# Optimization experiments

Hardware: AMD Instinct MI355X
Metric: run time of the kernel (lower is better)

## Reference

```python
import jax, jax.numpy as jnp
import numpy as np

jax.config.update("jax_enable_x64", True)

P = 2038074743          # prime used by the ROBE-Z hash
BLOCK_K = 32            # tile sizes of the hashed reconstruction (kernel tile)
BLOCK_N = 32
INPUT_DIM = 8192
OUTPUT_DIM = 8192
HASH_SIZE = 1 << 22     # compressed parameter count
TOKENS = 512


def setup_inputs() -> dict:
    key = jax.random.key(0)
    k1, k2 = jax.random.split(key, 2)
    x = jax.random.normal(k1, (TOKENS, INPUT_DIM), dtype=jnp.float32)
    hashed_weight = jax.random.normal(k2, (HASH_SIZE,), dtype=jnp.float32) * 0.02
    bias = jnp.zeros((OUTPUT_DIM,), dtype=jnp.float32)
    # mirrors RzLinear._generate_random_numbers(seed): 4 random ints made even, prepended with P
    rng = np.random.RandomState(1024)
    r = rng.randint(0, P, size=(4,)).astype(np.int64)
    r = r + (r % 2)
    random_numbers = jnp.asarray(np.concatenate([np.array([P], dtype=np.int64), r]), dtype=jnp.int64)
    return {"x": x, "hashed_weight": hashed_weight, "bias": bias, "random_numbers": random_numbers}


def _weight_indices(random_numbers):
    """Hashed flat indices into hashed_weight for the dense [K, N] weight."""
    K, N = INPUT_DIM, OUTPUT_DIM
    kt, nt = K // BLOCK_K, N // BLOCK_N
    R1, R2, R3 = random_numbers[1], random_numbers[2], random_numbers[3]
    k_ids = jnp.arange(kt, dtype=jnp.int64)
    n_ids = jnp.arange(nt, dtype=jnp.int64)
    # per-tile start offset into the compressed array
    start = ((k_ids[:, None] * R3 + n_ids[None, :] * R2 + R1) % P) % (HASH_SIZE - BLOCK_K * BLOCK_N + 1)
    start = start.astype(jnp.int32)  # [kt, nt]
    off = (jnp.arange(BLOCK_K, dtype=jnp.int32)[:, None] * BLOCK_N
           + jnp.arange(BLOCK_N, dtype=jnp.int32)[None, :])  # [BK, BN], row-major within tile
    idx = start[:, None, :, None] + off[None, :, None, :]    # [kt, BK, nt, BN]
    return idx.reshape(K, N)


def reference(x, hashed_weight, bias, random_numbers):
    idx = _weight_indices(random_numbers)          # [K, N] int32
    W = hashed_weight[idx]                          # hashed-gather reconstruction, [K, N]
    out = jnp.matmul(x, W) + bias[None, :]          # [tokens, N]
    return out
```

## Files before the change

### kernel.cpp

```cpp
#include <hip/hip_runtime.h>
#include <hip/hip_fp16.h>

#define NDIM 8192
#define KDIM 8192
#define NT 256
#define MOD2 4193281
#define PRIME 2038074743LL

#define BM 256
#define BN 128
#define BK 32
#define KITER 64
#define ASTRIDE 40
#define BSLAB 1032

typedef _Float16 half8 __attribute__((ext_vector_type(8)));
typedef float floatx4 __attribute__((ext_vector_type(4)));

__global__ __launch_bounds__(256) void prep_kernel(const float* __restrict__ x,
                                                   const float* __restrict__ hw,
                                                   const float* __restrict__ bias,
                                                   const int* __restrict__ rn,
                                                   __half* __restrict__ xh,
                                                   __half* __restrict__ hh,
                                                   int* __restrict__ starts,
                                                   float* __restrict__ out) {
    int b = blockIdx.x;
    int tid = threadIdx.x;
    if (b < 8192) {
        int i = b * 256 + tid;
        const float4* s; __half2* d; int j;
        if (i < (1 << 20)) { s = (const float4*)x;  d = (__half2*)xh; j = i; }
        else               { s = (const float4*)hw; d = (__half2*)hh; j = i - (1 << 20); }
        float4 v = s[j];
        d[j * 2]     = __floats2half2_rn(v.x, v.y);
        d[j * 2 + 1] = __floats2half2_rn(v.z, v.w);
    } else if (b < 8192 + 4096) {
        int i = (b - 8192) * 256 + tid;
        float4 bv = *(const float4*)(bias + ((i & 2047) << 2));
        ((float4*)out)[i] = bv;
    } else {
        int t = (b - 12288) * 256 + tid;
        bool is64 = (rn[1] == 0 && rn[3] == 0);
        long long R1 = is64 ? rn[2] : rn[1];
        long long R2 = is64 ? rn[4] : rn[2];
        long long R3 = is64 ? rn[6] : rn[3];
        long long k_id = t >> 8, n_id = t & 255;
        long long v = (k_id * R3 + n_id * R2 + R1) % PRIME;
        starts[t] = (int)(v % MOD2);
    }
}

__global__ __launch_bounds__(512, 4) void gemm_kernel(
    const __half* __restrict__ xh, const __half* __restrict__ hh,
    const int* __restrict__ starts, float* __restrict__ out) {
    __shared__ __align__(16) __half As[2][BM * ASTRIDE];
    __shared__ __align__(16) __half Bs[2][4 * BSLAB];
    __shared__ int Ss[KITER * 4];

    const int tid = threadIdx.x;
    const int lane = tid & 63;
    const int wave = tid >> 6;
    const int wm = wave >> 1;
    const int wn = wave & 1;
    const int quad = lane >> 4;
    const int l16 = lane & 15;

    const int i = blockIdx.x;
    const int ks = i & 3;
    const int m_blk = (i >> 2) & 1;
    const int n_blk = i >> 3;
    const int gm0 = m_blk * BM;
    const int gn0 = n_blk * BN;
    const int kt0 = ks * KITER;
    const int n_id0 = n_blk * 4;

    if (tid < KITER * 4) {
        int kp = tid >> 2, tile = tid & 3;
        Ss[tid] = starts[(kt0 + kp) * NT + n_id0 + tile];
    }

    const int a_row = tid >> 2;
    const int a_ch = tid & 3;
    const __half* aptr = xh + (size_t)(gm0 + a_row) * KDIM + kt0 * 32 + a_ch * 8;
    const unsigned a_woff = a_row * ASTRIDE + a_ch * 8;

    const int b_tile = tid >> 7;
    const int t7 = tid & 127;
    const int b_np = t7 & 15;
    const int b_kg = t7 >> 4;
    const int b_oct = b_kg >> 1;
    const unsigned b_woff = b_oct * BSLAB + (b_tile * 32 + 2 * b_np) * 8 + (b_kg & 1) * 4;

    uint4 paA0, paA1, paB0, paB1;
    unsigned pbA0, pbA1, pbA2, pbA3, pbB0, pbB1, pbB2, pbB3;

#define LOADT(P0, P1, Q0, Q1, Q2, Q3, kp_) do {                                \
        P0 = *(const uint4*)(aptr + (kp_) * 32);                               \
        P1 = *(const uint4*)(aptr + (size_t)128 * KDIM + (kp_) * 32);          \
        int st = Ss[(kp_) * 4 + b_tile];                                       \
        const __half* src = hh + st + b_kg * 128 + b_np * 2;                   \
        Q0 = *(const unsigned*)(src);                                          \
        Q1 = *(const unsigned*)(src + 32);                                     \
        Q2 = *(const unsigned*)(src + 64);                                     \
        Q3 = *(const unsigned*)(src + 96);                                     \
    } while (0)

#define STORET(P0, P1, Q0, Q1, Q2, Q3, buf_) do {                              \
        *(uint4*)&As[buf_][a_woff] = P0;                                       \
        *(uint4*)&As[buf_][(a_woff) + 128 * ASTRIDE] = P1;                     \
        unsigned lo0 = (Q0 & 0xffffu) | (Q1 << 16);                            \
        unsigned lo1 = (Q2 & 0xffffu) | (Q3 << 16);                            \
        unsigned hi0 = (Q0 >> 16) | (Q1 & 0xffff0000u);                        \
        unsigned hi1 = (Q2 >> 16) | (Q3 & 0xffff0000u);                        \
        uint2 e = {lo0, lo1}, o = {hi0, hi1};                                  \
        *(uint2*)&Bs[buf_][b_woff] = e;                                        \
        *(uint2*)&Bs[buf_][b_woff + 8] = o;                                    \
    } while (0)

    floatx4 acc[4][4];
#pragma unroll
    for (int r = 0; r < 4; r++)
#pragma unroll
        for (int c = 0; c < 4; c++)
            acc[r][c] = (floatx4){0.f, 0.f, 0.f, 0.f};

#define FRAGS_MFMA(buf_) do {                                                  \
        half8 af[4], bf[4];                                                    \
        _Pragma("unroll")                                                      \
        for (int r = 0; r < 4; r++)                                            \
            af[r] = *(const half8*)&As[buf_][(wm * 64 + r * 16 + l16) * ASTRIDE + quad * 8]; \
        _Pragma("unroll")                                                      \
        for (int c = 0; c < 4; c++)                                            \
            bf[c] = *(const half8*)&Bs[buf_][quad * BSLAB + (wn * 64 + c * 16 + l16) * 8];   \
        _Pragma("unroll")                                                      \
        for (int r = 0; r < 4; r++)                                            \
            _Pragma("unroll")                                                  \
            for (int c = 0; c < 4; c++)                                        \
                acc[r][c] = __builtin_amdgcn_mfma_f32_16x16x32_f16(af[r], bf[c], acc[r][c], 0, 0, 0); \
    } while (0)

    __syncthreads();
    LOADT(paA0, paA1, pbA0, pbA1, pbA2, pbA3, 0);
    LOADT(paB0, paB1, pbB0, pbB1, pbB2, pbB3, 1);
    STORET(paA0, paA1, pbA0, pbA1, pbA2, pbA3, 0);
    __syncthreads();

    for (int kp = 0; kp < KITER; kp += 2) {
        if (kp + 2 < KITER) LOADT(paA0, paA1, pbA0, pbA1, pbA2, pbA3, kp + 2);
        FRAGS_MFMA(0);
        STORET(paB0, paB1, pbB0, pbB1, pbB2, pbB3, 1);
        __syncthreads();

        if (kp + 3 < KITER) LOADT(paB0, paB1, pbB0, pbB1, pbB2, pbB3, kp + 3);
        FRAGS_MFMA(1);
        if (kp + 2 < KITER)
            STORET(paA0, paA1, pbA0, pbA1, pbA2, pbA3, 0);
        __syncthreads();
    }

#pragma unroll
    for (int c = 0; c < 4; c++) {
        int col = gn0 + wn * 64 + c * 16 + l16;
#pragma unroll
        for (int r = 0; r < 4; r++) {
            int row0 = gm0 + wm * 64 + r * 16 + quad * 4;
#pragma unroll
            for (int e = 0; e < 4; e++)
                atomicAdd(&out[(size_t)(row0 + e) * NDIM + col], acc[r][c][e]);
        }
    }
#undef LOADT
#undef STORET
#undef FRAGS_MFMA
}

extern "C" void kernel_launch(void* const* d_in, const int* in_sizes, int n_in,
                              void* d_out, int out_size, void* d_ws, size_t ws_size,
                              hipStream_t stream) {
    const float* x = (const float*)d_in[0];
    const float* hw = (const float*)d_in[1];
    const float* bias = (const float*)d_in[2];
    const int* rn = (const int*)d_in[3];
    float* out = (float*)d_out;

    char* ws = (char*)d_ws;
    __half* xh = (__half*)ws;
    __half* hh = (__half*)(ws + (8u << 20));
    int* starts = (int*)(ws + (16u << 20));

    hipLaunchKernelGGL(prep_kernel, dim3(12544), dim3(256), 0, stream,
                       x, hw, bias, rn, xh, hh, starts, out);
    hipLaunchKernelGGL(gemm_kernel, dim3(512), dim3(512), 0, stream, xh, hh, starts, out);
}
```

Measured before the change: 202.4 us.

## Fuse fp32-to-fp16 conversion and hash start computation into GEMM loads

Removes the separate pass that converts x and the hashed weight to fp16 and precomputes tile start offsets. The GEMM now loads fp32 directly, packs to half when storing to shared memory, and computes each block's hash starts inline. This drops a full read and write of about 24 MB of converted data, but doubles global load bytes in the GEMM main loop and raises register pressure for the prefetch buffers.

```diff
diff --git a/kernel.cpp b/kernel.cpp
--- a/kernel.cpp
+++ b/kernel.cpp
@@ -17,43 +17,26 @@
 typedef _Float16 half8 __attribute__((ext_vector_type(8)));
 typedef float floatx4 __attribute__((ext_vector_type(4)));
 
-__global__ __launch_bounds__(256) void prep_kernel(const float* __restrict__ x,
-                                                   const float* __restrict__ hw,
-                                                   const float* __restrict__ bias,
-                                                   const int* __restrict__ rn,
-                                                   __half* __restrict__ xh,
-                                                   __half* __restrict__ hh,
-                                                   int* __restrict__ starts,
+__global__ __launch_bounds__(256) void prep_kernel(const float* __restrict__ bias,
                                                    float* __restrict__ out) {
-    int b = blockIdx.x;
-    int tid = threadIdx.x;
-    if (b < 8192) {
-        int i = b * 256 + tid;
-        const float4* s; __half2* d; int j;
-        if (i < (1 << 20)) { s = (const float4*)x;  d = (__half2*)xh; j = i; }
-        else               { s = (const float4*)hw; d = (__half2*)hh; j = i - (1 << 20); }
-        float4 v = s[j];
-        d[j * 2]     = __floats2half2_rn(v.x, v.y);
-        d[j * 2 + 1] = __floats2half2_rn(v.z, v.w);
-    } else if (b < 8192 + 4096) {
-        int i = (b - 8192) * 256 + tid;
-        float4 bv = *(const float4*)(bias + ((i & 2047) << 2));
-        ((float4*)out)[i] = bv;
-    } else {
-        int t = (b - 12288) * 256 + tid;
-        bool is64 = (rn[1] == 0 && rn[3] == 0);
-        long long R1 = is64 ? rn[2] : rn[1];
-        long long R2 = is64 ? rn[4] : rn[2];
-        long long R3 = is64 ? rn[6] : rn[3];
-        long long k_id = t >> 8, n_id = t & 255;
-        long long v = (k_id * R3 + n_id * R2 + R1) % PRIME;
-        starts[t] = (int)(v % MOD2);
-    }
+    int i = blockIdx.x * 256 + threadIdx.x;
+    float4 bv = *(const float4*)(bias + ((i & 2047) << 2));
+    ((float4*)out)[i] = bv;
 }
 
+__device__ inline unsigned pkh(float a, float b) {
+    __half2 h = __floats2half2_rn(a, b);
+    return *reinterpret_cast<unsigned*>(&h);
+}
+
+struct PF {
+    float4 a0, a1, a2, a3;
+    float2 b0, b1, b2, b3;
+};
+
 __global__ __launch_bounds__(512, 4) void gemm_kernel(
-    const __half* __restrict__ xh, const __half* __restrict__ hh,
-    const int* __restrict__ starts, float* __restrict__ out) {
+    const float* __restrict__ x, const float* __restrict__ hw,
+    const int* __restrict__ rn, float* __restrict__ out) {
     __shared__ __align__(16) __half As[2][BM * ASTRIDE];
     __shared__ __align__(16) __half Bs[2][4 * BSLAB];
     __shared__ int Ss[KITER * 4];
@@ -77,12 +60,18 @@
 
     if (tid < KITER * 4) {
         int kp = tid >> 2, tile = tid & 3;
-        Ss[tid] = starts[(kt0 + kp) * NT + n_id0 + tile];
+        bool is64 = (rn[1] == 0 && rn[3] == 0);
+        long long R1 = is64 ? rn[2] : rn[1];
+        long long R2 = is64 ? rn[4] : rn[2];
+        long long R3 = is64 ? rn[6] : rn[3];
+        long long k_id = kt0 + kp, n_id = n_id0 + tile;
+        long long v = (k_id * R3 + n_id * R2 + R1) % PRIME;
+        Ss[tid] = (int)(v % MOD2);
     }
 
     const int a_row = tid >> 2;
     const int a_ch = tid & 3;
-    const __half* aptr = xh + (size_t)(gm0 + a_row) * KDIM + kt0 * 32 + a_ch * 8;
+    const float* aptr = x + (size_t)(gm0 + a_row) * KDIM + kt0 * 32 + a_ch * 8;
     const unsigned a_woff = a_row * ASTRIDE + a_ch * 8;
 
     const int b_tile = tid >> 7;
@@ -92,28 +81,30 @@
     const int b_oct = b_kg >> 1;
     const unsigned b_woff = b_oct * BSLAB + (b_tile * 32 + 2 * b_np) * 8 + (b_kg & 1) * 4;
 
-    uint4 paA0, paA1, paB0, paB1;
-    unsigned pbA0, pbA1, pbA2, pbA3, pbB0, pbB1, pbB2, pbB3;
+    PF pfA, pfB;
 
-#define LOADT(P0, P1, Q0, Q1, Q2, Q3, kp_) do {                                \
-        P0 = *(const uint4*)(aptr + (kp_) * 32);                               \
-        P1 = *(const uint4*)(aptr + (size_t)128 * KDIM + (kp_) * 32);          \
+#define LOADT(P, kp_) do {                                                     \
+        P.a0 = *(const float4*)(aptr + (kp_) * 32);                            \
+        P.a1 = *(const float4*)(aptr + (kp_) * 32 + 4);                        \
+        P.a2 = *(const float4*)(aptr + (size_t)128 * KDIM + (kp_) * 32);       \
+        P.a3 = *(const float4*)(aptr + (size_t)128 * KDIM + (kp_) * 32 + 4);   \
         int st = Ss[(kp_) * 4 + b_tile];                                       \
-        const __half* src = hh + st + b_kg * 128 + b_np * 2;                   \
-        Q0 = *(const unsigned*)(src);                                          \
-        Q1 = *(const unsigned*)(src + 32);                                     \
-        Q2 = *(const unsigned*)(src + 64);                                     \
-        Q3 = *(const unsigned*)(src + 96);                                     \
+        const float* src = hw + st + b_kg * 128 + b_np * 2;                    \
+        P.b0 = *(const float2*)(src);                                          \
+        P.b1 = *(const float2*)(src + 32);                                     \
+        P.b2 = *(const float2*)(src + 64);                                     \
+        P.b3 = *(const float2*)(src + 96);                                     \
     } while (0)
 
-#define STORET(P0, P1, Q0, Q1, Q2, Q3, buf_) do {                              \
-        *(uint4*)&As[buf_][a_woff] = P0;                                       \
-        *(uint4*)&As[buf_][(a_woff) + 128 * ASTRIDE] = P1;                     \
-        unsigned lo0 = (Q0 & 0xffffu) | (Q1 << 16);                            \
-        unsigned lo1 = (Q2 & 0xffffu) | (Q3 << 16);                            \
-        unsigned hi0 = (Q0 >> 16) | (Q1 & 0xffff0000u);                        \
-        unsigned hi1 = (Q2 >> 16) | (Q3 & 0xffff0000u);                        \
-        uint2 e = {lo0, lo1}, o = {hi0, hi1};                                  \
+#define STORET(P, buf_) do {                                                   \
+        uint4 av0 = { pkh(P.a0.x, P.a0.y), pkh(P.a0.z, P.a0.w),                \
+                      pkh(P.a1.x, P.a1.y), pkh(P.a1.z, P.a1.w) };              \
+        uint4 av1 = { pkh(P.a2.x, P.a2.y), pkh(P.a2.z, P.a2.w),                \
+                      pkh(P.a3.x, P.a3.y), pkh(P.a3.z, P.a3.w) };              \
+        *(uint4*)&As[buf_][a_woff] = av0;                                      \
+        *(uint4*)&As[buf_][a_woff + 128 * ASTRIDE] = av1;                      \
+        uint2 e = { pkh(P.b0.x, P.b1.x), pkh(P.b2.x, P.b3.x) };                \
+        uint2 o = { pkh(P.b0.y, P.b1.y), pkh(P.b2.y, P.b3.y) };                \
         *(uint2*)&Bs[buf_][b_woff] = e;                                        \
         *(uint2*)&Bs[buf_][b_woff + 8] = o;                                    \
     } while (0)
@@ -141,21 +132,21 @@
     } while (0)
 
     __syncthreads();
-    LOADT(paA0, paA1, pbA0, pbA1, pbA2, pbA3, 0);
-    LOADT(paB0, paB1, pbB0, pbB1, pbB2, pbB3, 1);
-    STORET(paA0, paA1, pbA0, pbA1, pbA2, pbA3, 0);
+    LOADT(pfA, 0);
+    LOADT(pfB, 1);
+    STORET(pfA, 0);
     __syncthreads();
 
     for (int kp = 0; kp < KITER; kp += 2) {
-        if (kp + 2 < KITER) LOADT(paA0, paA1, pbA0, pbA1, pbA2, pbA3, kp + 2);
+        if (kp + 2 < KITER) LOADT(pfA, kp + 2);
         FRAGS_MFMA(0);
-        STORET(paB0, paB1, pbB0, pbB1, pbB2, pbB3, 1);
+        STORET(pfB, 1);
         __syncthreads();
 
-        if (kp + 3 < KITER) LOADT(paB0, paB1, pbB0, pbB1, pbB2, pbB3, kp + 3);
+        if (kp + 3 < KITER) LOADT(pfB, kp + 3);
         FRAGS_MFMA(1);
         if (kp + 2 < KITER)
-            STORET(paA0, paA1, pbA0, pbA1, pbA2, pbA3, 0);
+            STORET(pfA, 0);
         __syncthreads();
     }
 
@@ -183,13 +174,8 @@
     const float* bias = (const float*)d_in[2];
     const int* rn = (const int*)d_in[3];
     float* out = (float*)d_out;
+    (void)d_ws; (void)ws_size;
 
-    char* ws = (char*)d_ws;
-    __half* xh = (__half*)ws;
-    __half* hh = (__half*)(ws + (8u << 20));
-    int* starts = (int*)(ws + (16u << 20));
-
-    hipLaunchKernelGGL(prep_kernel, dim3(12544), dim3(256), 0, stream,
-                       x, hw, bias, rn, xh, hh, starts, out);
-    hipLaunchKernelGGL(gemm_kernel, dim3(512), dim3(512), 0, stream, xh, hh, starts, out);
+    hipLaunchKernelGGL(prep_kernel, dim3(4096), dim3(256), 0, stream, bias, out);
+    hipLaunchKernelGGL(gemm_kernel, dim3(512), dim3(512), 0, stream, x, hw, rn, out);
 }
```

Result: slower. 410.6 us (+102.9%).

## Shrink GEMM block to 128x128 tile with 4 waves and 2-way split-K

Applied to the files above, without the earlier changes.

Reshapes the GEMM decomposition from 256x128 tiles with 8 waves and 4-way split-K to 128x128 tiles with 4 waves and 2-way split-K over 128 k-tiles each. Each thread now loads twice as many B elements per stage and the start-table prefetch loops over threads. The aim is to halve the atomicAdd traffic on the output and allow more resident blocks per CU. In exchange, each B tile is fetched by four M-blocks instead of two, and each block runs a longer serial K loop.

```diff
diff --git a/kernel.cpp b/kernel.cpp
--- a/kernel.cpp
+++ b/kernel.cpp
@@ -7,10 +7,10 @@
 #define MOD2 4193281
 #define PRIME 2038074743LL
 
-#define BM 256
+#define BM 128
 #define BN 128
 #define BK 32
-#define KITER 64
+#define KITER 128
 #define ASTRIDE 40
 #define BSLAB 1032
 
@@ -51,7 +51,7 @@
     }
 }
 
-__global__ __launch_bounds__(512, 4) void gemm_kernel(
+__global__ __launch_bounds__(256, 4) void gemm_kernel(
     const __half* __restrict__ xh, const __half* __restrict__ hh,
     const int* __restrict__ starts, float* __restrict__ out) {
     __shared__ __align__(16) __half As[2][BM * ASTRIDE];
@@ -67,17 +67,17 @@
     const int l16 = lane & 15;
 
     const int i = blockIdx.x;
-    const int ks = i & 3;
-    const int m_blk = (i >> 2) & 1;
+    const int ks = i & 1;
+    const int m_blk = (i >> 1) & 3;
     const int n_blk = i >> 3;
     const int gm0 = m_blk * BM;
     const int gn0 = n_blk * BN;
     const int kt0 = ks * KITER;
     const int n_id0 = n_blk * 4;
 
-    if (tid < KITER * 4) {
-        int kp = tid >> 2, tile = tid & 3;
-        Ss[tid] = starts[(kt0 + kp) * NT + n_id0 + tile];
+    for (int s = tid; s < KITER * 4; s += 256) {
+        int kp = s >> 2, tile = s & 3;
+        Ss[s] = starts[(kt0 + kp) * NT + n_id0 + tile];
     }
 
     const int a_row = tid >> 2;
@@ -85,37 +85,49 @@
     const __half* aptr = xh + (size_t)(gm0 + a_row) * KDIM + kt0 * 32 + a_ch * 8;
     const unsigned a_woff = a_row * ASTRIDE + a_ch * 8;
 
-    const int b_tile = tid >> 7;
-    const int t7 = tid & 127;
-    const int b_np = t7 & 15;
-    const int b_kg = t7 >> 4;
+    const int b_tile = tid >> 6;
+    const int t6 = tid & 63;
+    const int b_np = t6 & 15;
+    const int b_kg = t6 >> 4;
     const int b_oct = b_kg >> 1;
     const unsigned b_woff = b_oct * BSLAB + (b_tile * 32 + 2 * b_np) * 8 + (b_kg & 1) * 4;
 
     uint4 paA0, paA1, paB0, paB1;
-    unsigned pbA0, pbA1, pbA2, pbA3, pbB0, pbB1, pbB2, pbB3;
-
-#define LOADT(P0, P1, Q0, Q1, Q2, Q3, kp_) do {                                \
+    unsigned pbA0, pbA1, pbA2, pbA3, pbA4, pbA5, pbA6, pbA7;
+    unsigned pbB0, pbB1, pbB2, pbB3, pbB4, pbB5, pbB6, pbB7;
+
+#define LOADT(P0, P1, Q0, Q1, Q2, Q3, Q4, Q5, Q6, Q7, kp_) do {                \
         P0 = *(const uint4*)(aptr + (kp_) * 32);                               \
-        P1 = *(const uint4*)(aptr + (size_t)128 * KDIM + (kp_) * 32);          \
+        P1 = *(const uint4*)(aptr + (size_t)64 * KDIM + (kp_) * 32);           \
         int st = Ss[(kp_) * 4 + b_tile];                                       \
         const __half* src = hh + st + b_kg * 128 + b_np * 2;                   \
         Q0 = *(const unsigned*)(src);                                          \
         Q1 = *(const unsigned*)(src + 32);                                     \
         Q2 = *(const unsigned*)(src + 64);                                     \
         Q3 = *(const unsigned*)(src + 96);                                     \
+        Q4 = *(const unsigned*)(src + 512);                                    \
+        Q5 = *(const unsigned*)(src + 544);                                    \
+        Q6 = *(const unsigned*)(src + 576);                                    \
+        Q7 = *(const unsigned*)(src + 608);                                    \
     } while (0)
 
-#define STORET(P0, P1, Q0, Q1, Q2, Q3, buf_) do {                              \
+#define STORET(P0, P1, Q0, Q1, Q2, Q3, Q4, Q5, Q6, Q7, buf_) do {              \
         *(uint4*)&As[buf_][a_woff] = P0;                                       \
-        *(uint4*)&As[buf_][(a_woff) + 128 * ASTRIDE] = P1;                     \
+        *(uint4*)&As[buf_][(a_woff) + 64 * ASTRIDE] = P1;                      \
         unsigned lo0 = (Q0 & 0xffffu) | (Q1 << 16);                            \
         unsigned lo1 = (Q2 & 0xffffu) | (Q3 << 16);                            \
         unsigned hi0 = (Q0 >> 16) | (Q1 & 0xffff0000u);                        \
         unsigned hi1 = (Q2 >> 16) | (Q3 & 0xffff0000u);                        \
-        uint2 e = {lo0, lo1}, o = {hi0, hi1};                                  \
-        *(uint2*)&Bs[buf_][b_woff] = e;                                        \
-        *(uint2*)&Bs[buf_][b_woff + 8] = o;                                    \
+        uint2 e0 = {lo0, lo1}, o0 = {hi0, hi1};                                \
+        *(uint2*)&Bs[buf_][b_woff] = e0;                                       \
+        *(uint2*)&Bs[buf_][b_woff + 8] = o0;                                   \
+        unsigned lo2 = (Q4 & 0xffffu) | (Q5 << 16);                            \
+        unsigned lo3 = (Q6 & 0xffffu) | (Q7 << 16);                            \
+        unsigned hi2 = (Q4 >> 16) | (Q5 & 0xffff0000u);                        \
+        unsigned hi3 = (Q6 >> 16) | (Q7 & 0xffff0000u);                        \
+        uint2 e1 = {lo2, lo3}, o1 = {hi2, hi3};                                \
+        *(uint2*)&Bs[buf_][b_woff + 2 * BSLAB] = e1;                           \
+        *(uint2*)&Bs[buf_][b_woff + 2 * BSLAB + 8] = o1;                       \
     } while (0)
 
     floatx4 acc[4][4];
@@ -141,21 +153,23 @@
     } while (0)
 
     __syncthreads();
-    LOADT(paA0, paA1, pbA0, pbA1, pbA2, pbA3, 0);
-    LOADT(paB0, paB1, pbB0, pbB1, pbB2, pbB3, 1);
-    STORET(paA0, paA1, pbA0, pbA1, pbA2, pbA3, 0);
+    LOADT(paA0, paA1, pbA0, pbA1, pbA2, pbA3, pbA4, pbA5, pbA6, pbA7, 0);
+    LOADT(paB0, paB1, pbB0, pbB1, pbB2, pbB3, pbB4, pbB5, pbB6, pbB7, 1);
+    STORET(paA0, paA1, pbA0, pbA1, pbA2, pbA3, pbA4, pbA5, pbA6, pbA7, 0);
     __syncthreads();
 
     for (int kp = 0; kp < KITER; kp += 2) {
-        if (kp + 2 < KITER) LOADT(paA0, paA1, pbA0, pbA1, pbA2, pbA3, kp + 2);
+        if (kp + 2 < KITER)
+            LOADT(paA0, paA1, pbA0, pbA1, pbA2, pbA3, pbA4, pbA5, pbA6, pbA7, kp + 2);
         FRAGS_MFMA(0);
-        STORET(paB0, paB1, pbB0, pbB1, pbB2, pbB3, 1);
+        STORET(paB0, paB1, pbB0, pbB1, pbB2, pbB3, pbB4, pbB5, pbB6, pbB7, 1);
         __syncthreads();
 
-        if (kp + 3 < KITER) LOADT(paB0, paB1, pbB0, pbB1, pbB2, pbB3, kp + 3);
+        if (kp + 3 < KITER)
+            LOADT(paB0, paB1, pbB0, pbB1, pbB2, pbB3, pbB4, pbB5, pbB6, pbB7, kp + 3);
         FRAGS_MFMA(1);
         if (kp + 2 < KITER)
-            STORET(paA0, paA1, pbA0, pbA1, pbA2, pbA3, 0);
+            STORET(paA0, paA1, pbA0, pbA1, pbA2, pbA3, pbA4, pbA5, pbA6, pbA7, 0);
         __syncthreads();
     }
 
@@ -191,5 +205,5 @@
 
     hipLaunchKernelGGL(prep_kernel, dim3(12544), dim3(256), 0, stream,
                        x, hw, bias, rn, xh, hh, starts, out);
-    hipLaunchKernelGGL(gemm_kernel, dim3(512), dim3(512), 0, stream, xh, hh, starts, out);
+    hipLaunchKernelGGL(gemm_kernel, dim3(512), dim3(256), 0, stream, xh, hh, starts, out);
 }
```

After: 253.4 us. 25.2% more time.
